# Kernel tuning notes

Measured on AMD Instinct MI355X. Metric: run time of the kernel, lower is better.

Reference implementation:

```python
import jax, jax.numpy as jnp
import numpy as np

N = 50000
E = 1_600_000
IN_F = 128
OUT_F = 128
EMB = 3
KER = 4


def setup_inputs() -> dict:
    key = jax.random.key(0)
    k1, k2, k3, k4, k5 = jax.random.split(key, 5)
    x = jax.random.normal(k1, (N, IN_F), dtype=jnp.float32)
    edge_idx = jax.random.randint(k2, (2, E), 0, N, dtype=jnp.int64)
    # learned parameters (init mirrors reset_parameters, except sig=1.0 so
    # the Gaussian edge weights are non-degenerate)
    weight = 0.1 * jax.random.normal(k3, (IN_F, OUT_F, KER), dtype=jnp.float32)
    bias = 0.1 * jax.random.normal(k4, (OUT_F,), dtype=jnp.float32)
    mu = 0.005 * jax.random.normal(k5, (EMB, KER), dtype=jnp.float32)
    sig = jnp.ones((1, KER), dtype=jnp.float32)
    return {"x": x, "edge_idx": edge_idx, "weight": weight, "bias": bias, "mu": mu, "sig": sig}


def reference(x, edge_idx, weight, bias, mu, sig):
    n = x.shape[0]
    ker = weight.shape[2]
    row, col = edge_idx[0], edge_idx[1]
    domain = x[:, :3]                      # [N, 3]
    diff = domain[row] - domain[col]       # [E, 3]
    out = jnp.zeros((n, weight.shape[1]), dtype=x.dtype)
    for k in range(ker):                   # small fixed kernel loop (as in source)
        support = x @ weight[:, :, k]      # [N, out]
        # Gaussian edge weight: exp(sig_k * (-0.5 * ||diff - mu_k||^2))
        value = jnp.exp(sig[0, k] * (-0.5 * jnp.sum((diff - mu[:, k]) ** 2, axis=1)))  # [E]
        # sparse.mm(A, support): out[row] += value * support[col]
        msgs = value[:, None] * support[col]              # [E, out]
        out = out + jax.ops.segment_sum(msgs, row, num_segments=n)
    return out + bias
```

## Files before the change

kernel.cpp:

```cpp
#include <hip/hip_runtime.h>

#define IN_F 128
#define OUT_F 128
#define KER 4
#define CHUNK 16384

typedef unsigned int uint;
typedef unsigned short u16;
typedef __attribute__((ext_vector_type(8))) short bf16x8;
typedef __attribute__((ext_vector_type(4))) float f32x4;

__device__ __forceinline__ uint f2bf(float f) {
    uint u = __float_as_uint(f);
    u += 0x7fffu + ((u >> 16) & 1u);
    return u >> 16;
}


__global__ void __launch_bounds__(256) prep_kernel(
    const float* __restrict__ x, const float* __restrict__ weight,
    const float* __restrict__ mu, const float* __restrict__ sig, int n,
    u16* __restrict__ xbf, float4* __restrict__ dom, u16* __restrict__ W2p,
    float* __restrict__ kc, int nB1, int nB2) {
    const int b = blockIdx.x;
    if (b < nB1) {
        int t = b * 256 + threadIdx.x;
        if (t < n * 32) {
            float4 v = *reinterpret_cast<const float4*>(x + (size_t)t * 4);
            uint2 o;
            o.x = f2bf(v.x) | (f2bf(v.y) << 16);
            o.y = f2bf(v.z) | (f2bf(v.w) << 16);
            *reinterpret_cast<uint2*>(xbf + (size_t)t * 4) = o;
            if ((t & 31) == 0) dom[t >> 5] = make_float4(v.x, v.y, v.z, 0.f);
        }
    } else if (b < nB1 + nB2) {
        int t = (b - nB1) * 256 + threadIdx.x;
        if (t < 8192) {
            int lane = t & 63;
            int nfks = t >> 6;
            int ks = nfks & 15, nf = nfks >> 4;
            int f = nf * 16 + (lane & 15);
            int kbase = ks * 32 + ((lane >> 4) << 3);
            uint pk[4];
            #pragma unroll
            for (int jj = 0; jj < 4; ++jj) {
                int k0 = kbase + jj * 2;
                int c0 = k0 & 127, q0 = k0 >> 7;
                int k1 = k0 + 1;
                int c1 = k1 & 127, q1 = k1 >> 7;
                uint lo = f2bf(weight[((size_t)c0 * OUT_F + f) * KER + q0]);
                uint hi = f2bf(weight[((size_t)c1 * OUT_F + f) * KER + q1]);
                pk[jj] = lo | (hi << 16);
            }
            *reinterpret_cast<uint4*>(W2p + (size_t)t * 8) =
                make_uint4(pk[0], pk[1], pk[2], pk[3]);
        }
    } else {
        if (threadIdx.x < KER) {
            int k = threadIdx.x;
            float sg = sig[k];
            float m0 = mu[k], m1 = mu[KER + k], m2 = mu[2 * KER + k];
            kc[k * 5 + 0] = -0.5f * sg * (m0 * m0 + m1 * m1 + m2 * m2);
            kc[k * 5 + 1] = -0.5f * sg;
            kc[k * 5 + 2] = sg * m0;
            kc[k * 5 + 3] = sg * m1;
            kc[k * 5 + 4] = sg * m2;
        }
    }
}


__global__ void __launch_bounds__(1024) hist_kernel(
    const int* __restrict__ row, int E, int n, int nchunk,
    u16* __restrict__ hist) {
    extern __shared__ uint lds[];
    const int ch = blockIdx.x >> 2, q = blockIdx.x & 3;
    const int wq = (n + 3) >> 2;
    const int r_lo = q * wq;
    const int r_hi = min(n, r_lo + wq);
    const int width = r_hi - r_lo;
    const int words = (width + 1) >> 1;
    for (int i = threadIdx.x; i < words; i += 1024) lds[i] = 0;
    __syncthreads();
    const int base = ch * CHUNK;
    const int lim = min(base + CHUNK, E);
    for (int e = base + threadIdx.x; e < lim; e += 1024) {
        int r = row[e];
        if (r >= r_lo && r < r_hi) {
            int rr = r - r_lo;
            atomicAdd(&lds[rr >> 1], 1u << ((rr & 1) << 4));
        }
    }
    __syncthreads();
    uint* out32 = (uint*)(hist + (size_t)ch * n + r_lo);
    for (int i = threadIdx.x; i < words; i += 1024) out32[i] = lds[i];
}

__global__ void __launch_bounds__(256) colscan_kernel(
    const u16* __restrict__ hist, u16* __restrict__ bases,
    int* __restrict__ counts, int n, int nchunk) {
    int r = blockIdx.x * 256 + threadIdx.x;
    if (r >= n) return;
    uint acc = 0;
    for (int b = 0; b < nchunk; ++b) {
        uint t = hist[(size_t)b * n + r];
        bases[(size_t)b * n + r] = (u16)acc;
        acc += t;
    }
    counts[r] = (int)acc;
}

__global__ void scanA_kernel(const int* __restrict__ counts, int n, int* __restrict__ bsum) {
    __shared__ int wsum[16];
    int i = blockIdx.x * 1024 + threadIdx.x;
    int lane = threadIdx.x & 63, wv = threadIdx.x >> 6;
    int v = (i < n) ? counts[i] : 0;
    #pragma unroll
    for (int off = 32; off > 0; off >>= 1) v += __shfl_down(v, off, 64);
    if (lane == 0) wsum[wv] = v;
    __syncthreads();
    if (threadIdx.x == 0) {
        int t = 0;
        #pragma unroll
        for (int q = 0; q < 16; ++q) t += wsum[q];
        bsum[blockIdx.x] = t;
    }
}

__global__ void scanC_kernel(const int* __restrict__ counts, int n, const int* __restrict__ bsum,
                             int* __restrict__ row_ptr) {
    __shared__ int wsum[16];
    __shared__ int s_boff;
    const int tid = threadIdx.x, lane = tid & 63, wv = tid >> 6;
    const int i = blockIdx.x * 1024 + tid;
    if (tid < 64) {
        int v = (tid < blockIdx.x) ? bsum[tid] : 0;
        #pragma unroll
        for (int off = 32; off > 0; off >>= 1) v += __shfl_down(v, off, 64);
        if (tid == 0) s_boff = v;
    }
    int v = (i < n) ? counts[i] : 0;
    int s = v;
    #pragma unroll
    for (int off = 1; off < 64; off <<= 1) {
        int t = __shfl_up(s, off, 64);
        if (lane >= off) s += t;
    }
    if (lane == 63) wsum[wv] = s;
    __syncthreads();
    if (wv == 0 && lane < 16) {
        int w = wsum[lane];
        #pragma unroll
        for (int off = 1; off < 16; off <<= 1) {
            int t = __shfl_up(w, off, 64);
            if (lane >= off) w += t;
        }
        wsum[lane] = w;
    }
    __syncthreads();
    int base = s_boff + (wv ? wsum[wv - 1] : 0);
    int incl = base + s;
    if (i < n) row_ptr[i + 1] = incl;
    if (i == 0) row_ptr[0] = 0;
}

__global__ void __launch_bounds__(1024) place_kernel(
    const int* __restrict__ row, const int* __restrict__ col, int E, int n,
    const u16* __restrict__ bases, const int* __restrict__ row_ptr,
    const float4* __restrict__ dom, const float* __restrict__ kc,
    uint4* __restrict__ recs) {
    extern __shared__ uint lds[];
    const int ch = blockIdx.x >> 3, x = blockIdx.x & 7;
    const int wp = (n + 7) >> 3;
    const int r_lo = x * wp;
    const int r_hi = min(n, r_lo + wp);
    const int width = r_hi - r_lo;
    const int words = (width + 1) >> 1;
    for (int i = threadIdx.x; i < words; i += 1024) lds[i] = 0;
    __syncthreads();
    float A[4], B[4], C0[4], C1[4], C2[4];
    #pragma unroll
    for (int k = 0; k < 4; ++k) {
        A[k]  = kc[k * 5 + 0];
        B[k]  = kc[k * 5 + 1];
        C0[k] = kc[k * 5 + 2];
        C1[k] = kc[k * 5 + 3];
        C2[k] = kc[k * 5 + 4];
    }
    const int base = ch * CHUNK;
    const int lim = min(base + CHUNK, E);
    const u16* br = bases + (size_t)ch * n;
    for (int e = base + threadIdx.x; e < lim; e += 1024) {
        int r = row[e];
        if (r >= r_lo && r < r_hi) {
            int c = col[e];
            float4 dr = dom[r], dc = dom[c];
            float d0 = dr.x - dc.x, d1 = dr.y - dc.y, d2 = dr.z - dc.z;
            float S = fmaf(d2, d2, fmaf(d1, d1, d0 * d0));
            uint vb[4];
            #pragma unroll
            for (int k = 0; k < 4; ++k) {
                float t = fmaf(B[k], S, A[k]);
                t = fmaf(C0[k], d0, t);
                t = fmaf(C1[k], d1, t);
                t = fmaf(C2[k], d2, t);
                vb[k] = f2bf(__expf(t));
            }
            int rr = r - r_lo;
            uint sh = (rr & 1) << 4;
            uint old = atomicAdd(&lds[rr >> 1], 1u << sh);
            int rank = (int)((old >> sh) & 0xffffu);
            int pos = row_ptr[r] + (int)br[r] + rank;
            recs[pos] = make_uint4(vb[0] | (vb[1] << 16), vb[2] | (vb[3] << 16), (uint)c, 0u);
        }
    }
}


__global__ void __launch_bounds__(256) agg_kernel(
    const u16* __restrict__ xbf, const int* __restrict__ row_ptr,
    const uint4* __restrict__ recs, u16* __restrict__ aggbf, int n) {
    const int w = threadIdx.x >> 6, l = threadIdx.x & 63;
    const int i = blockIdx.x * 4 + w;
    if (i >= n) return;
    const int start = row_ptr[i];
    const int end   = row_ptr[i + 1];

    float acc[4][2];
    #pragma unroll
    for (int k = 0; k < 4; ++k) { acc[k][0] = 0.f; acc[k][1] = 0.f; }

    auto body = [&](uint lo, uint hi, uint xp) {
        float x0 = __uint_as_float(xp << 16);
        float x1 = __uint_as_float(xp & 0xffff0000u);
        float v0 = __uint_as_float(lo << 16);
        float v1 = __uint_as_float(lo & 0xffff0000u);
        float v2 = __uint_as_float(hi << 16);
        float v3 = __uint_as_float(hi & 0xffff0000u);
        acc[0][0] = fmaf(v0, x0, acc[0][0]); acc[0][1] = fmaf(v0, x1, acc[0][1]);
        acc[1][0] = fmaf(v1, x0, acc[1][0]); acc[1][1] = fmaf(v1, x1, acc[1][1]);
        acc[2][0] = fmaf(v2, x0, acc[2][0]); acc[2][1] = fmaf(v2, x1, acc[2][1]);
        acc[3][0] = fmaf(v3, x0, acc[3][0]); acc[3][1] = fmaf(v3, x1, acc[3][1]);
    };

    int j = start;
    for (; j + 4 <= end; j += 4) {
        uint4 r0 = recs[j + 0];
        uint4 r1 = recs[j + 1];
        uint4 r2 = recs[j + 2];
        uint4 r3 = recs[j + 3];
        uint xp0 = *reinterpret_cast<const uint*>(xbf + ((size_t)r0.z << 7) + (l << 1));
        uint xp1 = *reinterpret_cast<const uint*>(xbf + ((size_t)r1.z << 7) + (l << 1));
        uint xp2 = *reinterpret_cast<const uint*>(xbf + ((size_t)r2.z << 7) + (l << 1));
        uint xp3 = *reinterpret_cast<const uint*>(xbf + ((size_t)r3.z << 7) + (l << 1));
        body(r0.x, r0.y, xp0);
        body(r1.x, r1.y, xp1);
        body(r2.x, r2.y, xp2);
        body(r3.x, r3.y, xp3);
    }
    for (; j < end; ++j) {
        uint4 rc = recs[j];
        uint xp = *reinterpret_cast<const uint*>(xbf + ((size_t)rc.z << 7) + (l << 1));
        body(rc.x, rc.y, xp);
    }

    u16* o = aggbf + ((size_t)i << 9) + (l << 1);
    *reinterpret_cast<uint*>(o +   0) = f2bf(acc[0][0]) | (f2bf(acc[0][1]) << 16);
    *reinterpret_cast<uint*>(o + 128) = f2bf(acc[1][0]) | (f2bf(acc[1][1]) << 16);
    *reinterpret_cast<uint*>(o + 256) = f2bf(acc[2][0]) | (f2bf(acc[2][1]) << 16);
    *reinterpret_cast<uint*>(o + 384) = f2bf(acc[3][0]) | (f2bf(acc[3][1]) << 16);
}


__global__ void __launch_bounds__(256) gemm_kernel(
    const u16* __restrict__ aggbf, const u16* __restrict__ W2p,
    const float* __restrict__ bias, float* __restrict__ out, int n) {
    const int w = threadIdx.x >> 6, l = threadIdx.x & 63;
    const int r0 = blockIdx.x * 128 + w * 32;
    int ra = r0 + (l & 15);
    int rb = ra + 16;
    if (ra > n - 1) ra = n - 1;
    if (rb > n - 1) rb = n - 1;
    const u16* pa = aggbf + ((size_t)ra << 9) + ((l >> 4) << 3);
    const u16* pb = aggbf + ((size_t)rb << 9) + ((l >> 4) << 3);
    const u16* wp = W2p + ((size_t)l << 3);

    f32x4 acc[2][8];
    #pragma unroll
    for (int m = 0; m < 2; ++m)
        #pragma unroll
        for (int nf = 0; nf < 8; ++nf)
            acc[m][nf] = (f32x4){0.f, 0.f, 0.f, 0.f};

    #pragma unroll 2
    for (int ks = 0; ks < 16; ++ks) {
        bf16x8 a0 = *reinterpret_cast<const bf16x8*>(pa + ks * 32);
        bf16x8 a1 = *reinterpret_cast<const bf16x8*>(pb + ks * 32);
        #pragma unroll
        for (int nf = 0; nf < 8; ++nf) {
            bf16x8 bfr = *reinterpret_cast<const bf16x8*>(wp + (((nf << 4) + ks) << 9));
            acc[0][nf] = __builtin_amdgcn_mfma_f32_16x16x32_bf16(a0, bfr, acc[0][nf], 0, 0, 0);
            acc[1][nf] = __builtin_amdgcn_mfma_f32_16x16x32_bf16(a1, bfr, acc[1][nf], 0, 0, 0);
        }
    }

    const int cq = l >> 4;
    const int cr = l & 15;
    #pragma unroll
    for (int nf = 0; nf < 8; ++nf) {
        float bv = bias[(nf << 4) + cr];
        #pragma unroll
        for (int m = 0; m < 2; ++m) {
            #pragma unroll
            for (int rg = 0; rg < 4; ++rg) {
                int rowi = r0 + m * 16 + cq * 4 + rg;
                if (rowi < n)
                    out[(size_t)rowi * OUT_F + (nf << 4) + cr] = acc[m][nf][rg] + bv;
            }
        }
    }
}


extern "C" void kernel_launch(void* const* d_in, const int* in_sizes, int n_in,
                              void* d_out, int out_size, void* d_ws, size_t ws_size,
                              hipStream_t stream) {
    const float* x      = (const float*)d_in[0];
    const int*   edge   = (const int*)d_in[1];
    const float* weight = (const float*)d_in[2];
    const float* bias   = (const float*)d_in[3];
    const float* mu     = (const float*)d_in[4];
    const float* sig    = (const float*)d_in[5];
    float* out = (float*)d_out;

    const int n = in_sizes[0] / IN_F;
    const int E = in_sizes[1] / 2;
    const int* row = edge;
    const int* col = edge + E;
    const int nchunk = (E + CHUNK - 1) / CHUNK;

    char* ws = (char*)d_ws;
    size_t off = 0;
    auto alloc = [&](size_t bytes) {
        size_t o = off;
        off = (off + bytes + 255) & ~(size_t)255;
        return o;
    };
    u16*    xbf        = (u16*)(ws + alloc((size_t)n * IN_F * 2));
    float4* dom        = (float4*)(ws + alloc((size_t)n * 16));
    uint4*  recs       = (uint4*)(ws + alloc((size_t)E * 16));
    u16*    aggbf      = (u16*)(ws + alloc((size_t)n * KER * IN_F * 2));
    u16*    W2p        = (u16*)(ws + alloc((size_t)KER * IN_F * OUT_F * 2));
    u16*    hist       = (u16*)(ws + alloc((size_t)nchunk * n * 2));
    u16*    bases      = (u16*)(ws + alloc((size_t)nchunk * n * 2));
    int*    counts     = (int*)(ws + alloc((size_t)n * 4));
    int*    row_ptr    = (int*)(ws + alloc(((size_t)n + 1) * 4));
    int*    bsum       = (int*)(ws + alloc(1024 * 4));
    float*  kc         = (float*)(ws + alloc(32 * 4));
    if (off > ws_size) return;

    const int nB1 = (n * 32 + 255) / 256;
    const int nB2 = 32;
    prep_kernel<<<nB1 + nB2 + 1, 256, 0, stream>>>(x, weight, mu, sig, n, xbf, dom, W2p,
                                                   kc, nB1, nB2);
    const int wq = (n + 3) >> 2;
    const size_t hist_lds = (size_t)((wq + 1) >> 1) * 4;
    hist_kernel<<<nchunk * 4, 1024, hist_lds, stream>>>(row, E, n, nchunk, hist);
    colscan_kernel<<<(n + 255) / 256, 256, 0, stream>>>(hist, bases, counts, n, nchunk);
    const int nb = (n + 1023) / 1024;
    scanA_kernel<<<nb, 1024, 0, stream>>>(counts, n, bsum);
    scanC_kernel<<<nb, 1024, 0, stream>>>(counts, n, bsum, row_ptr);
    const int wp = (n + 7) >> 3;
    const size_t place_lds = (size_t)((wp + 1) >> 1) * 4;
    place_kernel<<<nchunk * 8, 1024, place_lds, stream>>>(row, col, E, n, bases, row_ptr,
                                                          dom, kc, recs);
    agg_kernel<<<(n + 3) / 4, 256, 0, stream>>>(xbf, row_ptr, recs, aggbf, n);
    gemm_kernel<<<(n + 127) / 128, 256, 0, stream>>>(aggbf, W2p, bias, out, n);
}
```

Baseline: 295.6 us.

## Fuse aggregation with GEMM, merge scan kernels, precompute positions, enlarge chunks

Aggregation and the dense projection now run in one kernel. Each block aggregates 16 rows into a swizzled LDS tile and then runs MFMA over it, so the n×512 bf16 intermediate no longer goes through global memory. The block-sum scan is folded into colscan using atomics, and scanC precomputes per-chunk absolute positions so place does one lookup per edge. The place loop is unrolled 4 ways for memory-level parallelism. CHUNK is doubled and hist uses 2 row partitions instead of 4, which cuts the launch count but adds a posbase array and makes W2p reloads per block more frequent.

Result: faster. 281.9 us (-4.7%).

```diff
diff --git a/kernel.cpp b/kernel.cpp
--- a/kernel.cpp
+++ b/kernel.cpp
@@ -3,7 +3,7 @@
 #define IN_F 128
 #define OUT_F 128
 #define KER 4
-#define CHUNK 16384
+#define CHUNK 32768
 
 typedef unsigned int uint;
 typedef unsigned short u16;
@@ -21,7 +21,7 @@
     const float* __restrict__ x, const float* __restrict__ weight,
     const float* __restrict__ mu, const float* __restrict__ sig, int n,
     u16* __restrict__ xbf, float4* __restrict__ dom, u16* __restrict__ W2p,
-    float* __restrict__ kc, int nB1, int nB2) {
+    float* __restrict__ kc, int* __restrict__ bsum, int nB1, int nB2) {
     const int b = blockIdx.x;
     if (b < nB1) {
         int t = b * 256 + threadIdx.x;
@@ -66,16 +66,17 @@
             kc[k * 5 + 3] = sg * m1;
             kc[k * 5 + 4] = sg * m2;
         }
+        if (threadIdx.x >= 64 && threadIdx.x < 128) bsum[threadIdx.x - 64] = 0;
     }
 }
 
 
 __global__ void __launch_bounds__(1024) hist_kernel(
-    const int* __restrict__ row, int E, int n, int nchunk,
+    const int* __restrict__ row, int E, int n,
     u16* __restrict__ hist) {
     extern __shared__ uint lds[];
-    const int ch = blockIdx.x >> 2, q = blockIdx.x & 3;
-    const int wq = (n + 3) >> 2;
+    const int ch = blockIdx.x >> 1, q = blockIdx.x & 1;
+    const int wq = (n + 1) >> 1;
     const int r_lo = q * wq;
     const int r_hi = min(n, r_lo + wq);
     const int width = r_hi - r_lo;
@@ -84,6 +85,7 @@
     __syncthreads();
     const int base = ch * CHUNK;
     const int lim = min(base + CHUNK, E);
+    #pragma unroll 4
     for (int e = base + threadIdx.x; e < lim; e += 1024) {
         int r = row[e];
         if (r >= r_lo && r < r_hi) {
@@ -98,37 +100,31 @@
 
 __global__ void __launch_bounds__(256) colscan_kernel(
     const u16* __restrict__ hist, u16* __restrict__ bases,
-    int* __restrict__ counts, int n, int nchunk) {
+    int* __restrict__ counts, int* __restrict__ bsum, int n, int nchunk) {
+    __shared__ int red[4];
     int r = blockIdx.x * 256 + threadIdx.x;
-    if (r >= n) return;
     uint acc = 0;
-    for (int b = 0; b < nchunk; ++b) {
-        uint t = hist[(size_t)b * n + r];
-        bases[(size_t)b * n + r] = (u16)acc;
-        acc += t;
-    }
-    counts[r] = (int)acc;
-}
-
-__global__ void scanA_kernel(const int* __restrict__ counts, int n, int* __restrict__ bsum) {
-    __shared__ int wsum[16];
-    int i = blockIdx.x * 1024 + threadIdx.x;
+    if (r < n) {
+        for (int b = 0; b < nchunk; ++b) {
+            uint t = hist[(size_t)b * n + r];
+            bases[(size_t)b * n + r] = (u16)acc;
+            acc += t;
+        }
+        counts[r] = (int)acc;
+    }
     int lane = threadIdx.x & 63, wv = threadIdx.x >> 6;
-    int v = (i < n) ? counts[i] : 0;
+    int v = (r < n) ? (int)acc : 0;
     #pragma unroll
     for (int off = 32; off > 0; off >>= 1) v += __shfl_down(v, off, 64);
-    if (lane == 0) wsum[wv] = v;
-    __syncthreads();
-    if (threadIdx.x == 0) {
-        int t = 0;
-        #pragma unroll
-        for (int q = 0; q < 16; ++q) t += wsum[q];
-        bsum[blockIdx.x] = t;
-    }
+    if (lane == 0) red[wv] = v;
+    __syncthreads();
+    if (threadIdx.x == 0)
+        atomicAdd(&bsum[blockIdx.x >> 2], red[0] + red[1] + red[2] + red[3]);
 }
 
 __global__ void scanC_kernel(const int* __restrict__ counts, int n, const int* __restrict__ bsum,
-                             int* __restrict__ row_ptr) {
+                             const u16* __restrict__ bases, int* __restrict__ posbase,
+                             int* __restrict__ row_ptr, int nchunk) {
     __shared__ int wsum[16];
     __shared__ int s_boff;
     const int tid = threadIdx.x, lane = tid & 63, wv = tid >> 6;
@@ -160,15 +156,19 @@
     __syncthreads();
     int base = s_boff + (wv ? wsum[wv - 1] : 0);
     int incl = base + s;
-    if (i < n) row_ptr[i + 1] = incl;
+    if (i < n) {
+        row_ptr[i + 1] = incl;
+        int rp0 = incl - v;
+        for (int ch = 0; ch < nchunk; ++ch)
+            posbase[(size_t)ch * n + i] = rp0 + (int)bases[(size_t)ch * n + i];
+    }
     if (i == 0) row_ptr[0] = 0;
 }
 
 __global__ void __launch_bounds__(1024) place_kernel(
     const int* __restrict__ row, const int* __restrict__ col, int E, int n,
-    const u16* __restrict__ bases, const int* __restrict__ row_ptr,
-    const float4* __restrict__ dom, const float* __restrict__ kc,
-    uint4* __restrict__ recs) {
+    const int* __restrict__ posbase, const float4* __restrict__ dom,
+    const float* __restrict__ kc, uint4* __restrict__ recs) {
     extern __shared__ uint lds[];
     const int ch = blockIdx.x >> 3, x = blockIdx.x & 7;
     const int wp = (n + 7) >> 3;
@@ -189,13 +189,26 @@
     }
     const int base = ch * CHUNK;
     const int lim = min(base + CHUNK, E);
-    const u16* br = bases + (size_t)ch * n;
-    for (int e = base + threadIdx.x; e < lim; e += 1024) {
-        int r = row[e];
-        if (r >= r_lo && r < r_hi) {
-            int c = col[e];
-            float4 dr = dom[r], dc = dom[c];
-            float d0 = dr.x - dc.x, d1 = dr.y - dc.y, d2 = dr.z - dc.z;
+    const int* pb = posbase + (size_t)ch * n;
+    for (int e0 = base + threadIdx.x; e0 < lim; e0 += 4096) {
+        int rr[4], cc[4];
+        bool act[4];
+        #pragma unroll
+        for (int u = 0; u < 4; ++u) {
+            int e = e0 + u * 1024;
+            bool inb = e < lim;
+            rr[u] = inb ? row[e] : 0;
+            cc[u] = inb ? col[e] : 0;
+            act[u] = inb && (rr[u] >= r_lo) && (rr[u] < r_hi);
+        }
+        float4 drv[4], dcv[4];
+        #pragma unroll
+        for (int u = 0; u < 4; ++u)
+            if (act[u]) { drv[u] = dom[rr[u]]; dcv[u] = dom[cc[u]]; }
+        #pragma unroll
+        for (int u = 0; u < 4; ++u) {
+            if (!act[u]) continue;
+            float d0 = drv[u].x - dcv[u].x, d1 = drv[u].y - dcv[u].y, d2 = drv[u].z - dcv[u].z;
             float S = fmaf(d2, d2, fmaf(d1, d1, d0 * d0));
             uint vb[4];
             #pragma unroll
@@ -206,117 +219,107 @@
                 t = fmaf(C2[k], d2, t);
                 vb[k] = f2bf(__expf(t));
             }
-            int rr = r - r_lo;
-            uint sh = (rr & 1) << 4;
-            uint old = atomicAdd(&lds[rr >> 1], 1u << sh);
+            int rl = rr[u] - r_lo;
+            uint sh = (rl & 1) << 4;
+            uint old = atomicAdd(&lds[rl >> 1], 1u << sh);
             int rank = (int)((old >> sh) & 0xffffu);
-            int pos = row_ptr[r] + (int)br[r] + rank;
-            recs[pos] = make_uint4(vb[0] | (vb[1] << 16), vb[2] | (vb[3] << 16), (uint)c, 0u);
-        }
-    }
-}
-
-
-__global__ void __launch_bounds__(256) agg_kernel(
+            int pos = pb[rr[u]] + rank;
+            recs[pos] = make_uint4(vb[0] | (vb[1] << 16), vb[2] | (vb[3] << 16),
+                                   (uint)cc[u], 0u);
+        }
+    }
+}
+
+
+__global__ void __launch_bounds__(256) aggemm_kernel(
     const u16* __restrict__ xbf, const int* __restrict__ row_ptr,
-    const uint4* __restrict__ recs, u16* __restrict__ aggbf, int n) {
+    const uint4* __restrict__ recs, const u16* __restrict__ W2p,
+    const float* __restrict__ bias, float* __restrict__ out, int n) {
+    __shared__ u16 tile[16 * 512];
     const int w = threadIdx.x >> 6, l = threadIdx.x & 63;
-    const int i = blockIdx.x * 4 + w;
-    if (i >= n) return;
-    const int start = row_ptr[i];
-    const int end   = row_ptr[i + 1];
-
-    float acc[4][2];
+    const int rbase = blockIdx.x * 16;
+
+    for (int q = 0; q < 4; ++q) {
+        const int lr = w * 4 + q;
+        const int i = rbase + lr;
+        float acc[4][2];
+        #pragma unroll
+        for (int k = 0; k < 4; ++k) { acc[k][0] = 0.f; acc[k][1] = 0.f; }
+        if (i < n) {
+            const int start = row_ptr[i];
+            const int end   = row_ptr[i + 1];
+            auto body = [&](uint lo, uint hi, uint xp) {
+                float x0 = __uint_as_float(xp << 16);
+                float x1 = __uint_as_float(xp & 0xffff0000u);
+                float v0 = __uint_as_float(lo << 16);
+                float v1 = __uint_as_float(lo & 0xffff0000u);
+                float v2 = __uint_as_float(hi << 16);
+                float v3 = __uint_as_float(hi & 0xffff0000u);
+                acc[0][0] = fmaf(v0, x0, acc[0][0]); acc[0][1] = fmaf(v0, x1, acc[0][1]);
+                acc[1][0] = fmaf(v1, x0, acc[1][0]); acc[1][1] = fmaf(v1, x1, acc[1][1]);
+                acc[2][0] = fmaf(v2, x0, acc[2][0]); acc[2][1] = fmaf(v2, x1, acc[2][1]);
+                acc[3][0] = fmaf(v3, x0, acc[3][0]); acc[3][1] = fmaf(v3, x1, acc[3][1]);
+            };
+            int j = start;
+            for (; j + 4 <= end; j += 4) {
+                uint4 r0 = recs[j + 0];
+                uint4 r1 = recs[j + 1];
+                uint4 r2 = recs[j + 2];
+                uint4 r3 = recs[j + 3];
+                uint xp0 = *reinterpret_cast<const uint*>(xbf + ((size_t)r0.z << 7) + (l << 1));
+                uint xp1 = *reinterpret_cast<const uint*>(xbf + ((size_t)r1.z << 7) + (l << 1));
+                uint xp2 = *reinterpret_cast<const uint*>(xbf + ((size_t)r2.z << 7) + (l << 1));
+                uint xp3 = *reinterpret_cast<const uint*>(xbf + ((size_t)r3.z << 7) + (l << 1));
+                body(r0.x, r0.y, xp0);
+                body(r1.x, r1.y, xp1);
+                body(r2.x, r2.y, xp2);
+                body(r3.x, r3.y, xp3);
+            }
+            for (; j < end; ++j) {
+                uint4 rc = recs[j];
+                uint xp = *reinterpret_cast<const uint*>(xbf + ((size_t)rc.z << 7) + (l << 1));
+                body(rc.x, rc.y, xp);
+            }
+        }
+        const int swz = (lr & 7) << 4;
+        #pragma unroll
+        for (int k = 0; k < 4; ++k) {
+            int byte = lr * 1024 + k * 256 + (l << 2);
+            byte ^= swz;
+            *reinterpret_cast<uint*>((char*)tile + byte) =
+                f2bf(acc[k][0]) | (f2bf(acc[k][1]) << 16);
+        }
+    }
+    __syncthreads();
+
+    f32x4 c2[2];
+    c2[0] = (f32x4){0.f, 0.f, 0.f, 0.f};
+    c2[1] = (f32x4){0.f, 0.f, 0.f, 0.f};
+    const u16* wpb = W2p + ((size_t)l << 3);
+    const int arow = l & 15;
+    const int aswz = (arow & 7) << 4;
+    #pragma unroll 4
+    for (int ks = 0; ks < 16; ++ks) {
+        int byte = arow * 1024 + ks * 64 + ((l >> 4) << 4);
+        byte ^= aswz;
+        bf16x8 a = *reinterpret_cast<const bf16x8*>((char*)tile + byte);
+        #pragma unroll
+        for (int nf2 = 0; nf2 < 2; ++nf2) {
+            int nf = w * 2 + nf2;
+            bf16x8 b = *reinterpret_cast<const bf16x8*>(wpb + (((size_t)((nf << 4) + ks)) << 9));
+            c2[nf2] = __builtin_amdgcn_mfma_f32_16x16x32_bf16(a, b, c2[nf2], 0, 0, 0);
+        }
+    }
+    const int cq = l >> 4, cr = l & 15;
     #pragma unroll
-    for (int k = 0; k < 4; ++k) { acc[k][0] = 0.f; acc[k][1] = 0.f; }
-
-    auto body = [&](uint lo, uint hi, uint xp) {
-        float x0 = __uint_as_float(xp << 16);
-        float x1 = __uint_as_float(xp & 0xffff0000u);
-        float v0 = __uint_as_float(lo << 16);
-        float v1 = __uint_as_float(lo & 0xffff0000u);
-        float v2 = __uint_as_float(hi << 16);
-        float v3 = __uint_as_float(hi & 0xffff0000u);
-        acc[0][0] = fmaf(v0, x0, acc[0][0]); acc[0][1] = fmaf(v0, x1, acc[0][1]);
-        acc[1][0] = fmaf(v1, x0, acc[1][0]); acc[1][1] = fmaf(v1, x1, acc[1][1]);
-        acc[2][0] = fmaf(v2, x0, acc[2][0]); acc[2][1] = fmaf(v2, x1, acc[2][1]);
-        acc[3][0] = fmaf(v3, x0, acc[3][0]); acc[3][1] = fmaf(v3, x1, acc[3][1]);
-    };
-
-    int j = start;
-    for (; j + 4 <= end; j += 4) {
-        uint4 r0 = recs[j + 0];
-        uint4 r1 = recs[j + 1];
-        uint4 r2 = recs[j + 2];
-        uint4 r3 = recs[j + 3];
-        uint xp0 = *reinterpret_cast<const uint*>(xbf + ((size_t)r0.z << 7) + (l << 1));
-        uint xp1 = *reinterpret_cast<const uint*>(xbf + ((size_t)r1.z << 7) + (l << 1));
-        uint xp2 = *reinterpret_cast<const uint*>(xbf + ((size_t)r2.z << 7) + (l << 1));
-        uint xp3 = *reinterpret_cast<const uint*>(xbf + ((size_t)r3.z << 7) + (l << 1));
-        body(r0.x, r0.y, xp0);
-        body(r1.x, r1.y, xp1);
-        body(r2.x, r2.y, xp2);
-        body(r3.x, r3.y, xp3);
-    }
-    for (; j < end; ++j) {
-        uint4 rc = recs[j];
-        uint xp = *reinterpret_cast<const uint*>(xbf + ((size_t)rc.z << 7) + (l << 1));
-        body(rc.x, rc.y, xp);
-    }
-
-    u16* o = aggbf + ((size_t)i << 9) + (l << 1);
-    *reinterpret_cast<uint*>(o +   0) = f2bf(acc[0][0]) | (f2bf(acc[0][1]) << 16);
-    *reinterpret_cast<uint*>(o + 128) = f2bf(acc[1][0]) | (f2bf(acc[1][1]) << 16);
-    *reinterpret_cast<uint*>(o + 256) = f2bf(acc[2][0]) | (f2bf(acc[2][1]) << 16);
-    *reinterpret_cast<uint*>(o + 384) = f2bf(acc[3][0]) | (f2bf(acc[3][1]) << 16);
-}
-
-
-__global__ void __launch_bounds__(256) gemm_kernel(
-    const u16* __restrict__ aggbf, const u16* __restrict__ W2p,
-    const float* __restrict__ bias, float* __restrict__ out, int n) {
-    const int w = threadIdx.x >> 6, l = threadIdx.x & 63;
-    const int r0 = blockIdx.x * 128 + w * 32;
-    int ra = r0 + (l & 15);
-    int rb = ra + 16;
-    if (ra > n - 1) ra = n - 1;
-    if (rb > n - 1) rb = n - 1;
-    const u16* pa = aggbf + ((size_t)ra << 9) + ((l >> 4) << 3);
-    const u16* pb = aggbf + ((size_t)rb << 9) + ((l >> 4) << 3);
-    const u16* wp = W2p + ((size_t)l << 3);
-
-    f32x4 acc[2][8];
-    #pragma unroll
-    for (int m = 0; m < 2; ++m)
-        #pragma unroll
-        for (int nf = 0; nf < 8; ++nf)
-            acc[m][nf] = (f32x4){0.f, 0.f, 0.f, 0.f};
-
-    #pragma unroll 2
-    for (int ks = 0; ks < 16; ++ks) {
-        bf16x8 a0 = *reinterpret_cast<const bf16x8*>(pa + ks * 32);
-        bf16x8 a1 = *reinterpret_cast<const bf16x8*>(pb + ks * 32);
-        #pragma unroll
-        for (int nf = 0; nf < 8; ++nf) {
-            bf16x8 bfr = *reinterpret_cast<const bf16x8*>(wp + (((nf << 4) + ks) << 9));
-            acc[0][nf] = __builtin_amdgcn_mfma_f32_16x16x32_bf16(a0, bfr, acc[0][nf], 0, 0, 0);
-            acc[1][nf] = __builtin_amdgcn_mfma_f32_16x16x32_bf16(a1, bfr, acc[1][nf], 0, 0, 0);
-        }
-    }
-
-    const int cq = l >> 4;
-    const int cr = l & 15;
-    #pragma unroll
-    for (int nf = 0; nf < 8; ++nf) {
-        float bv = bias[(nf << 4) + cr];
-        #pragma unroll
-        for (int m = 0; m < 2; ++m) {
-            #pragma unroll
-            for (int rg = 0; rg < 4; ++rg) {
-                int rowi = r0 + m * 16 + cq * 4 + rg;
-                if (rowi < n)
-                    out[(size_t)rowi * OUT_F + (nf << 4) + cr] = acc[m][nf][rg] + bv;
-            }
+    for (int nf2 = 0; nf2 < 2; ++nf2) {
+        int colf = (w * 2 + nf2) * 16 + cr;
+        float bv = bias[colf];
+        #pragma unroll
+        for (int j = 0; j < 4; ++j) {
+            int rowi = rbase + cq * 4 + j;
+            if (rowi < n)
+                out[(size_t)rowi * OUT_F + colf] = c2[nf2][j] + bv;
         }
     }
 }
@@ -346,34 +349,32 @@
         off = (off + bytes + 255) & ~(size_t)255;
         return o;
     };
-    u16*    xbf        = (u16*)(ws + alloc((size_t)n * IN_F * 2));
-    float4* dom        = (float4*)(ws + alloc((size_t)n * 16));
-    uint4*  recs       = (uint4*)(ws + alloc((size_t)E * 16));
-    u16*    aggbf      = (u16*)(ws + alloc((size_t)n * KER * IN_F * 2));
-    u16*    W2p        = (u16*)(ws + alloc((size_t)KER * IN_F * OUT_F * 2));
-    u16*    hist       = (u16*)(ws + alloc((size_t)nchunk * n * 2));
-    u16*    bases      = (u16*)(ws + alloc((size_t)nchunk * n * 2));
-    int*    counts     = (int*)(ws + alloc((size_t)n * 4));
-    int*    row_ptr    = (int*)(ws + alloc(((size_t)n + 1) * 4));
-    int*    bsum       = (int*)(ws + alloc(1024 * 4));
-    float*  kc         = (float*)(ws + alloc(32 * 4));
+    u16*    xbf      = (u16*)(ws + alloc((size_t)n * IN_F * 2));
+    float4* dom      = (float4*)(ws + alloc((size_t)n * 16));
+    uint4*  recs     = (uint4*)(ws + alloc((size_t)E * 16));
+    u16*    W2p      = (u16*)(ws + alloc((size_t)KER * IN_F * OUT_F * 2));
+    u16*    hist     = (u16*)(ws + alloc((size_t)nchunk * n * 2));
+    u16*    bases    = (u16*)(ws + alloc((size_t)nchunk * n * 2));
+    int*    posbase  = (int*)(ws + alloc((size_t)nchunk * n * 4));
+    int*    counts   = (int*)(ws + alloc((size_t)n * 4));
+    int*    row_ptr  = (int*)(ws + alloc(((size_t)n + 1) * 4));
+    int*    bsum     = (int*)(ws + alloc(1024 * 4));
+    float*  kc       = (float*)(ws + alloc(32 * 4));
     if (off > ws_size) return;
 
     const int nB1 = (n * 32 + 255) / 256;
     const int nB2 = 32;
     prep_kernel<<<nB1 + nB2 + 1, 256, 0, stream>>>(x, weight, mu, sig, n, xbf, dom, W2p,
-                                                   kc, nB1, nB2);
-    const int wq = (n + 3) >> 2;
+                                                   kc, bsum, nB1, nB2);
+    const int wq = (n + 1) >> 1;
     const size_t hist_lds = (size_t)((wq + 1) >> 1) * 4;
-    hist_kernel<<<nchunk * 4, 1024, hist_lds, stream>>>(row, E, n, nchunk, hist);
-    colscan_kernel<<<(n + 255) / 256, 256, 0, stream>>>(hist, bases, counts, n, nchunk);
+    hist_kernel<<<nchunk * 2, 1024, hist_lds, stream>>>(row, E, n, hist);
+    colscan_kernel<<<(n + 255) / 256, 256, 0, stream>>>(hist, bases, counts, bsum, n, nchunk);
     const int nb = (n + 1023) / 1024;
-    scanA_kernel<<<nb, 1024, 0, stream>>>(counts, n, bsum);
-    scanC_kernel<<<nb, 1024, 0, stream>>>(counts, n, bsum, row_ptr);
+    scanC_kernel<<<nb, 1024, 0, stream>>>(counts, n, bsum, bases, posbase, row_ptr, nchunk);
     const int wp = (n + 7) >> 3;
     const size_t place_lds = (size_t)((wp + 1) >> 1) * 4;
-    place_kernel<<<nchunk * 8, 1024, place_lds, stream>>>(row, col, E, n, bases, row_ptr,
+    place_kernel<<<nchunk * 8, 1024, place_lds, stream>>>(row, col, E, n, posbase,
                                                           dom, kc, recs);
-    agg_kernel<<<(n + 3) / 4, 256, 0, stream>>>(xbf, row_ptr, recs, aggbf, n);
-    gemm_kernel<<<(n + 127) / 128, 256, 0, stream>>>(aggbf, W2p, bias, out, n);
-}
+    aggemm_kernel<<<(n + 15) / 16, 256, 0, stream>>>(xbf, row_ptr, recs, W2p, bias, out, n);
+}
```
